# Kernel optimization log

Hardware: AMD Instinct MI355X
Metric: run time of the kernel (lower is better)

The kernel has to match this reference:

```python
import jax, jax.numpy as jnp
import numpy as np

B, S, D = 2, 2048, 1024
H, HD = 16, 64


def setup_inputs() -> dict:
    key = jax.random.key(0)
    ks = jax.random.split(key, 6)
    hidden_states = jax.random.normal(ks[0], (B, S, D), dtype=jnp.float32)
    c_attn_w = jax.random.normal(ks[1], (D, 3 * D), dtype=jnp.float32) * 0.02
    c_attn_b = jnp.zeros((3 * D,), dtype=jnp.float32)
    c_proj_w = jax.random.normal(ks[2], (D, D), dtype=jnp.float32) * 0.02
    c_proj_b = jnp.zeros((D,), dtype=jnp.float32)
    basis = jax.random.normal(ks[3], (H, HD, HD), dtype=jnp.float32) * 0.1
    projectors = jnp.einsum('hdr,her->hde', basis, basis)  # basis @ basis.T per head
    return {
        'hidden_states': hidden_states,
        'c_attn_w': c_attn_w,
        'c_attn_b': c_attn_b,
        'c_proj_w': c_proj_w,
        'c_proj_b': c_proj_b,
        'projectors': projectors,
    }


def reference(hidden_states, c_attn_w, c_attn_b, c_proj_w, c_proj_b, projectors):
    # GPT2 Conv1D: out = x @ W + b
    qkv = hidden_states @ c_attn_w + c_attn_b  # [B,S,3D]
    q, k, v = jnp.split(qkv, 3, axis=-1)
    # split heads -> [B,H,S,HD]
    def split_heads(t):
        return t.reshape(B, S, H, HD).transpose(0, 2, 1, 3)
    q, k, v = split_heads(q), split_heads(k), split_heads(v)
    scores = jnp.einsum('bhqd,bhkd->bhqk', q, k) / jnp.sqrt(jnp.float32(HD))
    causal = jnp.tril(jnp.ones((S, S), dtype=bool))
    scores = jnp.where(causal, scores, jnp.finfo(scores.dtype).min)
    probs = jax.nn.softmax(scores, axis=-1)
    attn = jnp.einsum('bhqk,bhkd->bhqd', probs, v)  # [B,H,S,HD]
    # per-head basis projector applied to attention output
    attn = jnp.einsum('bhsd,hde->bhse', attn, projectors)
    # merge heads -> [B,S,D]
    attn = attn.transpose(0, 2, 1, 3).reshape(B, S, D)
    out = attn @ c_proj_w + c_proj_b
    return out
```

## Files before the change

### kernel.cpp

```cpp
#include <hip/hip_runtime.h>

typedef __attribute__((ext_vector_type(8))) short bhalf8;
typedef __attribute__((ext_vector_type(4))) float f32x4;
typedef __attribute__((ext_vector_type(8))) unsigned short u16x8;
typedef __attribute__((ext_vector_type(4))) unsigned short u16x4;

#define BDIM 2
#define SDIM 2048
#define DDIM 1024
#define HDIM 16
#define HDHD 64

__device__ __forceinline__ unsigned short f2bf(float f) {
  unsigned u = __builtin_bit_cast(unsigned, f);
  u += 0x7fffu + ((u >> 16) & 1u);
  return (unsigned short)(u >> 16);
}

__global__ __launch_bounds__(256) void cvt_hidden(const float* __restrict__ x,
                                                  unsigned short* __restrict__ y) {
  size_t i = ((size_t)blockIdx.x * 256 + threadIdx.x) * 4;
  f32x4 v = *(const f32x4*)(x + i);
  u16x4 o;
  o[0] = f2bf(v[0]); o[1] = f2bf(v[1]); o[2] = f2bf(v[2]); o[3] = f2bf(v[3]);
  *(u16x4*)(y + i) = o;
}

__global__ __launch_bounds__(256) void transpose_cvt(const float* __restrict__ W,
                                                     unsigned short* __restrict__ Wt,
                                                     int R, int C) {
  __shared__ float tl[32][33];
  int rt = blockIdx.x * 32, ct = blockIdx.y * 32;
  int r8 = threadIdx.x >> 5, c = threadIdx.x & 31;
#pragma unroll
  for (int i = 0; i < 4; i++)
    tl[r8 + i * 8][c] = W[(size_t)(rt + r8 + i * 8) * C + ct + c];
  __syncthreads();
#pragma unroll
  for (int i = 0; i < 4; i++)
    Wt[(size_t)(ct + r8 + i * 8) * R + rt + c] = f2bf(tl[c][r8 + i * 8]);
}

__global__ __launch_bounds__(256) void make_wproj(const float* __restrict__ proj,
                                                  const float* __restrict__ wproj,
                                                  unsigned short* __restrict__ WT) {
  int h = blockIdx.x, ot = blockIdx.y * 64;
  __shared__ float Pl[64][65];
  __shared__ float Wl[64][65];
  int t = threadIdx.x;
#pragma unroll
  for (int i = 0; i < 16; i++) {
    int idx = t + 256 * i;
    int a = idx >> 6, bc = idx & 63;
    Pl[a][bc] = proj[(size_t)h * 4096 + idx];
    Wl[a][bc] = wproj[(size_t)(h * 64 + a) * 1024 + ot + bc];
  }
  __syncthreads();
  int d = t & 63, ob = t >> 6;
#pragma unroll
  for (int i = 0; i < 16; i++) {
    int o = ob + i * 4;
    float acc = 0.f;
#pragma unroll
    for (int e = 0; e < 64; e++) acc += Pl[d][e] * Wl[e][o];
    WT[(size_t)(ot + o) * 1024 + h * 64 + d] = f2bf(acc);
  }
}

template <int EPI>
__global__ __launch_bounds__(256) void gemm_bt(
    const unsigned short* __restrict__ A, const unsigned short* __restrict__ Bt,
    const float* __restrict__ bias, float* __restrict__ Cf,
    unsigned short* __restrict__ q, unsigned short* __restrict__ k,
    unsigned short* __restrict__ v, int M, int N, int K) {
  __shared__ unsigned short As[128][72];
  __shared__ unsigned short Bs[128][72];
  const int tid = threadIdx.x;
  const int m0 = blockIdx.y * 128, n0 = blockIdx.x * 128;
  f32x4 acc[4][4];
#pragma unroll
  for (int m = 0; m < 4; m++)
#pragma unroll
    for (int n = 0; n < 4; n++) acc[m][n] = f32x4{0.f, 0.f, 0.f, 0.f};
  const int w = tid >> 6, lane = tid & 63;
  const int wr = (w >> 1) * 64, wc = (w & 1) * 64;
  const int lrow = lane & 15, lk = (lane >> 4) * 8;

  for (int kt = 0; kt < K; kt += 64) {
    __syncthreads();
#pragma unroll
    for (int i = 0; i < 4; i++) {
      int cch = tid + 256 * i;
      int r = cch >> 3, c8 = cch & 7;
      *(u16x8*)(&As[r][c8 * 8]) = *(const u16x8*)(A + (size_t)(m0 + r) * K + kt + c8 * 8);
      *(u16x8*)(&Bs[r][c8 * 8]) = *(const u16x8*)(Bt + (size_t)(n0 + r) * K + kt + c8 * 8);
    }
    __syncthreads();
#pragma unroll
    for (int kk = 0; kk < 2; kk++) {
      bhalf8 af[4], bfr[4];
#pragma unroll
      for (int m = 0; m < 4; m++) af[m] = *(const bhalf8*)(&As[wr + m * 16 + lrow][kk * 32 + lk]);
#pragma unroll
      for (int n = 0; n < 4; n++) bfr[n] = *(const bhalf8*)(&Bs[wc + n * 16 + lrow][kk * 32 + lk]);
#pragma unroll
      for (int m = 0; m < 4; m++)
#pragma unroll
        for (int n = 0; n < 4; n++)
          acc[m][n] = __builtin_amdgcn_mfma_f32_16x16x32_bf16(af[m], bfr[n], acc[m][n], 0, 0, 0);
    }
  }
  const int g = lane >> 4, il = lane & 15;
#pragma unroll
  for (int m = 0; m < 4; m++) {
    int rowb = wr + m * 16 + 4 * g;
#pragma unroll
    for (int n = 0; n < 4; n++) {
      int col = n0 + wc + n * 16 + il;
      float bs = bias[col];
#pragma unroll
      for (int r = 0; r < 4; r++) {
        int row = m0 + rowb + r;
        float val = acc[m][n][r] + bs;
        if (EPI == 0) {
          int which = col >> 10, hh = (col >> 6) & 15, hd = col & 63;
          int b = row >> 11, s = row & 2047;
          size_t idx = ((size_t)(b * 16 + hh) * SDIM + s) * HDHD + hd;
          unsigned short bv = f2bf(which == 0 ? val * 0.1803368801f : val);
          if (which == 0) q[idx] = bv;
          else if (which == 1) k[idx] = bv;
          else v[idx] = bv;
        } else {
          Cf[(size_t)row * N + col] = val;
        }
      }
    }
  }
}

__global__ __launch_bounds__(128, 2) void attn_kernel(const unsigned short* __restrict__ Q,
                                                      const unsigned short* __restrict__ Kb,
                                                      const unsigned short* __restrict__ Vb,
                                                      unsigned short* __restrict__ Om) {
  __shared__ unsigned short Ks[64][72];
  __shared__ unsigned short Vt[64][72];
  __shared__ unsigned short Ps[2][32][72];
  const int bh = blockIdx.x;
  const int qt = 31 - blockIdx.y;
  const int tid = threadIdx.x;
  const int w = tid >> 6, lane = tid & 63;
  const int g = lane >> 4, il = lane & 15;
  const int qbase = qt * 64 + w * 32;
  const size_t bhS = (size_t)bh * SDIM;

  bhalf8 qf[2][2];
#pragma unroll
  for (int f = 0; f < 2; f++) {
    const unsigned short* qp = Q + (bhS + qbase + f * 16 + il) * HDHD + g * 8;
    qf[f][0] = *(const bhalf8*)(qp);
    qf[f][1] = *(const bhalf8*)(qp + 32);
  }
  f32x4 oacc[2][4];
#pragma unroll
  for (int f = 0; f < 2; f++)
#pragma unroll
    for (int i = 0; i < 4; i++) oacc[f][i] = f32x4{0.f, 0.f, 0.f, 0.f};
  float mrun[2] = {-1e30f, -1e30f}, lrun[2] = {0.f, 0.f};

  const int krow = tid >> 1;
  const int kchk = (tid & 1) * 32;
  const int vd0 = (tid & 31) * 2;
  const int vkg = (tid >> 5) * 16;
  const int nt = qt + 1;

  for (int kt = 0; kt < nt; kt++) {
    const size_t kbase = (bhS + (size_t)kt * 64) * HDHD;
    __syncthreads();
    {
      const unsigned short* src = Kb + kbase + krow * HDHD + kchk;
      *(u16x8*)(&Ks[krow][kchk]) = *(const u16x8*)(src);
      *(u16x8*)(&Ks[krow][kchk + 8]) = *(const u16x8*)(src + 8);
      *(u16x8*)(&Ks[krow][kchk + 16]) = *(const u16x8*)(src + 16);
      *(u16x8*)(&Ks[krow][kchk + 24]) = *(const u16x8*)(src + 24);
    }
    {
      const unsigned short* vsrc = Vb + kbase + (size_t)vkg * HDHD + vd0;
      u16x8 lo0, lo1, hi0, hi1;
#pragma unroll
      for (int i = 0; i < 8; i++) {
        unsigned vv = *(const unsigned*)(vsrc + i * HDHD);
        lo0[i] = (unsigned short)(vv & 0xffffu); hi0[i] = (unsigned short)(vv >> 16);
      }
#pragma unroll
      for (int i = 0; i < 8; i++) {
        unsigned vv = *(const unsigned*)(vsrc + (8 + i) * HDHD);
        lo1[i] = (unsigned short)(vv & 0xffffu); hi1[i] = (unsigned short)(vv >> 16);
      }
      *(u16x8*)(&Vt[vd0][vkg]) = lo0;     *(u16x8*)(&Vt[vd0][vkg + 8]) = lo1;
      *(u16x8*)(&Vt[vd0 + 1][vkg]) = hi0; *(u16x8*)(&Vt[vd0 + 1][vkg + 8]) = hi1;
    }
    __syncthreads();
    f32x4 s[2][4];
#pragma unroll
    for (int f = 0; f < 2; f++)
#pragma unroll
      for (int c = 0; c < 4; c++) s[f][c] = f32x4{0.f, 0.f, 0.f, 0.f};
#pragma unroll
    for (int c = 0; c < 4; c++) {
      bhalf8 kf0 = *(const bhalf8*)(&Ks[c * 16 + il][g * 8]);
      bhalf8 kf1 = *(const bhalf8*)(&Ks[c * 16 + il][32 + g * 8]);
#pragma unroll
      for (int f = 0; f < 2; f++) {
        s[f][c] = __builtin_amdgcn_mfma_f32_16x16x32_bf16(kf0, qf[f][0], s[f][c], 0, 0, 0);
        s[f][c] = __builtin_amdgcn_mfma_f32_16x16x32_bf16(kf1, qf[f][1], s[f][c], 0, 0, 0);
      }
    }
    const bool diag = (kt == qt);
#pragma unroll
    for (int f = 0; f < 2; f++) {
      const int thr = w * 32 + f * 16 + il;
      float p[4][4];
      float lmax = -1e30f;
#pragma unroll
      for (int c = 0; c < 4; c++)
#pragma unroll
        for (int r = 0; r < 4; r++) {
          float v = s[f][c][r];
          if (diag && (c * 16 + 4 * g + r > thr)) v = -1e30f;
          p[c][r] = v;
          lmax = fmaxf(lmax, v);
        }
      lmax = fmaxf(lmax, __shfl_xor(lmax, 16));
      lmax = fmaxf(lmax, __shfl_xor(lmax, 32));
      float mn = fmaxf(mrun[f], lmax);
      float sc = exp2f(mrun[f] - mn);
      mrun[f] = mn;
      float rs = 0.f;
#pragma unroll
      for (int c = 0; c < 4; c++)
#pragma unroll
        for (int r = 0; r < 4; r++) { p[c][r] = exp2f(p[c][r] - mn); rs += p[c][r]; }
      rs += __shfl_xor(rs, 16);
      rs += __shfl_xor(rs, 32);
      lrun[f] = lrun[f] * sc + rs;
#pragma unroll
      for (int df = 0; df < 4; df++)
#pragma unroll
        for (int r = 0; r < 4; r++) oacc[f][df][r] *= sc;
#pragma unroll
      for (int c = 0; c < 4; c++) {
        u16x4 pk;
#pragma unroll
        for (int r = 0; r < 4; r++) pk[r] = f2bf(p[c][r]);
        *(u16x4*)(&Ps[w][f * 16 + il][c * 16 + 4 * g]) = pk;
      }
    }
#pragma unroll
    for (int kk = 0; kk < 2; kk++) {
      bhalf8 pf0 = *(const bhalf8*)(&Ps[w][il][kk * 32 + g * 8]);
      bhalf8 pf1 = *(const bhalf8*)(&Ps[w][16 + il][kk * 32 + g * 8]);
#pragma unroll
      for (int df = 0; df < 4; df++) {
        bhalf8 vf = *(const bhalf8*)(&Vt[df * 16 + il][kk * 32 + g * 8]);
        oacc[0][df] = __builtin_amdgcn_mfma_f32_16x16x32_bf16(vf, pf0, oacc[0][df], 0, 0, 0);
        oacc[1][df] = __builtin_amdgcn_mfma_f32_16x16x32_bf16(vf, pf1, oacc[1][df], 0, 0, 0);
      }
    }
  }
  __syncthreads();
#pragma unroll
  for (int f = 0; f < 2; f++) {
    float inv = 1.f / lrun[f];
#pragma unroll
    for (int df = 0; df < 4; df++) {
      u16x4 o;
#pragma unroll
      for (int r = 0; r < 4; r++) o[r] = f2bf(oacc[f][df][r] * inv);
      *(u16x4*)(&Ks[w * 32 + f * 16 + il][df * 16 + 4 * g]) = o;
    }
  }
  __syncthreads();
  {
    const int row = tid >> 1, half = (tid & 1) * 32;
    const int b = bh >> 4, h = bh & 15;
    size_t obase = ((size_t)b * SDIM + qt * 64 + row) * DDIM + h * HDHD + half;
#pragma unroll
    for (int c8 = 0; c8 < 4; c8++)
      *(u16x8*)(Om + obase + c8 * 8) = *(const u16x8*)(&Ks[row][half + c8 * 8]);
  }
}

extern "C" void kernel_launch(void* const* d_in, const int* in_sizes, int n_in,
                              void* d_out, int out_size, void* d_ws, size_t ws_size,
                              hipStream_t stream) {
  const float* hidden = (const float*)d_in[0];
  const float* attn_w = (const float*)d_in[1];
  const float* attn_b = (const float*)d_in[2];
  const float* proj_w = (const float*)d_in[3];
  const float* proj_b = (const float*)d_in[4];
  const float* projectors = (const float*)d_in[5];
  float* out = (float*)d_out;
  char* ws = (char*)d_ws;
  (void)in_sizes; (void)n_in; (void)out_size; (void)ws_size;

  unsigned short* hseq   = (unsigned short*)(ws);
  unsigned short* wqkvT  = (unsigned short*)(ws + 8388608);
  unsigned short* qb     = (unsigned short*)(ws + 14680064);
  unsigned short* kb     = (unsigned short*)(ws + 23068672);
  unsigned short* vb     = (unsigned short*)(ws + 31457280);
  unsigned short* attnM  = (unsigned short*)(ws + 39845888);
  unsigned short* wprojT = (unsigned short*)(ws + 48234496);

  cvt_hidden<<<dim3(4096), dim3(256), 0, stream>>>(hidden, hseq);
  transpose_cvt<<<dim3(32, 96), dim3(256), 0, stream>>>(attn_w, wqkvT, 1024, 3072);
  make_wproj<<<dim3(16, 16), dim3(256), 0, stream>>>(projectors, proj_w, wprojT);
  gemm_bt<0><<<dim3(24, 32), dim3(256), 0, stream>>>(hseq, wqkvT, attn_b, nullptr,
                                                     qb, kb, vb, 4096, 3072, 1024);
  attn_kernel<<<dim3(32, 32), dim3(128), 0, stream>>>(qb, kb, vb, attnM);
  gemm_bt<1><<<dim3(8, 32), dim3(256), 0, stream>>>(attnM, wprojT, proj_b, out,
                                                    nullptr, nullptr, nullptr, 4096, 1024, 1024);
}
```

Baseline: 177.2 us.

## Split causal attention over key segments with a separate reduction pass

Attention is split along the key dimension into segments of 8 key tiles, launched as a 3D grid, so the long diagonal query tiles no longer dominate and the workload is balanced across CUs. Each segment writes bf16 partial outputs with per-row max/sum, and a new reduce kernel combines them. The partial kernel also prefetches the next K/V tile into registers and raises the occupancy hint. The cost is an extra launch, a workspace round-trip, and bf16 rounding of the partials; the old single-pass kernel remains as a fallback when the workspace is too small.

```diff
diff --git a/kernel.cpp b/kernel.cpp
--- a/kernel.cpp
+++ b/kernel.cpp
@@ -15,6 +15,9 @@
   unsigned u = __builtin_bit_cast(unsigned, f);
   u += 0x7fffu + ((u >> 16) & 1u);
   return (unsigned short)(u >> 16);
+}
+__device__ __forceinline__ float bf2f(unsigned short u) {
+  return __builtin_bit_cast(float, (unsigned)u << 16);
 }
 
 __global__ __launch_bounds__(256) void cvt_hidden(const float* __restrict__ x,
@@ -138,7 +141,237 @@
   }
 }
 
-__global__ __launch_bounds__(128, 2) void attn_kernel(const unsigned short* __restrict__ Q,
+__global__ __launch_bounds__(128, 3) void attn_partial(const unsigned short* __restrict__ Q,
+                                                       const unsigned short* __restrict__ Kb,
+                                                       const unsigned short* __restrict__ Vb,
+                                                       unsigned short* __restrict__ PO,
+                                                       float2* __restrict__ ML) {
+  __shared__ unsigned short Ks[64][72];
+  __shared__ unsigned short Vt[64][72];
+  __shared__ unsigned short Ps[2][32][72];
+  const int bh = blockIdx.x;
+  const int qt = 31 - blockIdx.y;
+  const int seg = blockIdx.z;
+  const int a = qt >> 3, bq = qt & 7;
+  const int nseg = a + 1;
+  if (seg >= nseg) return;
+  const int k0 = seg * 8;
+  const int k1 = min(k0 + 8, qt + 1);
+
+  const int tid = threadIdx.x;
+  const int w = tid >> 6, lane = tid & 63;
+  const int g = lane >> 4, il = lane & 15;
+  const int qbase = qt * 64 + w * 32;
+  const size_t bhS = (size_t)bh * SDIM;
+
+  bhalf8 qf[2][2];
+#pragma unroll
+  for (int f = 0; f < 2; f++) {
+    const unsigned short* qp = Q + (bhS + qbase + f * 16 + il) * HDHD + g * 8;
+    qf[f][0] = *(const bhalf8*)(qp);
+    qf[f][1] = *(const bhalf8*)(qp + 32);
+  }
+  f32x4 oacc[2][4];
+#pragma unroll
+  for (int f = 0; f < 2; f++)
+#pragma unroll
+    for (int i = 0; i < 4; i++) oacc[f][i] = f32x4{0.f, 0.f, 0.f, 0.f};
+  float mrun[2] = {-1e30f, -1e30f}, lrun[2] = {0.f, 0.f};
+
+  const int krow = tid >> 1;
+  const int kchk = (tid & 1) * 32;
+  const int vd0 = (tid & 31) * 2;
+  const int vkg = (tid >> 5) * 16;
+
+  u16x8 kr[4];
+  unsigned vr[16];
+  {
+    const size_t kb0 = (bhS + (size_t)k0 * 64) * HDHD;
+    const unsigned short* ksrc = Kb + kb0 + krow * HDHD + kchk;
+#pragma unroll
+    for (int i = 0; i < 4; i++) kr[i] = *(const u16x8*)(ksrc + i * 8);
+    const unsigned short* vsrc = Vb + kb0 + (size_t)vkg * HDHD + vd0;
+#pragma unroll
+    for (int i = 0; i < 16; i++) vr[i] = *(const unsigned*)(vsrc + i * HDHD);
+  }
+
+  for (int kt = k0; kt < k1; kt++) {
+    __syncthreads();
+#pragma unroll
+    for (int i = 0; i < 4; i++) *(u16x8*)(&Ks[krow][kchk + i * 8]) = kr[i];
+    {
+      u16x8 lo0, lo1, hi0, hi1;
+#pragma unroll
+      for (int i = 0; i < 8; i++) {
+        lo0[i] = (unsigned short)(vr[i] & 0xffffu); hi0[i] = (unsigned short)(vr[i] >> 16);
+      }
+#pragma unroll
+      for (int i = 0; i < 8; i++) {
+        lo1[i] = (unsigned short)(vr[8 + i] & 0xffffu); hi1[i] = (unsigned short)(vr[8 + i] >> 16);
+      }
+      *(u16x8*)(&Vt[vd0][vkg]) = lo0;     *(u16x8*)(&Vt[vd0][vkg + 8]) = lo1;
+      *(u16x8*)(&Vt[vd0 + 1][vkg]) = hi0; *(u16x8*)(&Vt[vd0 + 1][vkg + 8]) = hi1;
+    }
+    if (kt + 1 < k1) {
+      const size_t kbn = (bhS + (size_t)(kt + 1) * 64) * HDHD;
+      const unsigned short* ksrc = Kb + kbn + krow * HDHD + kchk;
+#pragma unroll
+      for (int i = 0; i < 4; i++) kr[i] = *(const u16x8*)(ksrc + i * 8);
+      const unsigned short* vsrc = Vb + kbn + (size_t)vkg * HDHD + vd0;
+#pragma unroll
+      for (int i = 0; i < 16; i++) vr[i] = *(const unsigned*)(vsrc + i * HDHD);
+    }
+    __syncthreads();
+    f32x4 s[2][4];
+#pragma unroll
+    for (int f = 0; f < 2; f++)
+#pragma unroll
+      for (int c = 0; c < 4; c++) s[f][c] = f32x4{0.f, 0.f, 0.f, 0.f};
+#pragma unroll
+    for (int c = 0; c < 4; c++) {
+      bhalf8 kf0 = *(const bhalf8*)(&Ks[c * 16 + il][g * 8]);
+      bhalf8 kf1 = *(const bhalf8*)(&Ks[c * 16 + il][32 + g * 8]);
+#pragma unroll
+      for (int f = 0; f < 2; f++) {
+        s[f][c] = __builtin_amdgcn_mfma_f32_16x16x32_bf16(kf0, qf[f][0], s[f][c], 0, 0, 0);
+        s[f][c] = __builtin_amdgcn_mfma_f32_16x16x32_bf16(kf1, qf[f][1], s[f][c], 0, 0, 0);
+      }
+    }
+    const bool diag = (kt == qt);
+    float lmax[2];
+#pragma unroll
+    for (int f = 0; f < 2; f++) {
+      const int thr = w * 32 + f * 16 + il;
+      float lm = -1e30f;
+#pragma unroll
+      for (int c = 0; c < 4; c++)
+#pragma unroll
+        for (int r = 0; r < 4; r++) {
+          float v = s[f][c][r];
+          if (diag && (c * 16 + 4 * g + r > thr)) v = -1e30f;
+          s[f][c][r] = v;
+          lm = fmaxf(lm, v);
+        }
+      lm = fmaxf(lm, __shfl_xor(lm, 16));
+      lm = fmaxf(lm, __shfl_xor(lm, 32));
+      lmax[f] = lm;
+    }
+    if (!__all((lmax[0] <= mrun[0] + 7.f) && (lmax[1] <= mrun[1] + 7.f))) {
+#pragma unroll
+      for (int f = 0; f < 2; f++) {
+        float mn = fmaxf(mrun[f], lmax[f]);
+        float sc = exp2f(mrun[f] - mn);
+        mrun[f] = mn;
+        lrun[f] *= sc;
+#pragma unroll
+        for (int df = 0; df < 4; df++)
+#pragma unroll
+          for (int r = 0; r < 4; r++) oacc[f][df][r] *= sc;
+      }
+    }
+#pragma unroll
+    for (int f = 0; f < 2; f++) {
+      float rs = 0.f;
+#pragma unroll
+      for (int c = 0; c < 4; c++) {
+        u16x4 pk;
+#pragma unroll
+        for (int r = 0; r < 4; r++) {
+          float pv = exp2f(s[f][c][r] - mrun[f]);
+          rs += pv;
+          pk[r] = f2bf(pv);
+        }
+        *(u16x4*)(&Ps[w][f * 16 + il][c * 16 + 4 * g]) = pk;
+      }
+      rs += __shfl_xor(rs, 16);
+      rs += __shfl_xor(rs, 32);
+      lrun[f] += rs;
+    }
+#pragma unroll
+    for (int kk = 0; kk < 2; kk++) {
+      bhalf8 pf0 = *(const bhalf8*)(&Ps[w][il][kk * 32 + g * 8]);
+      bhalf8 pf1 = *(const bhalf8*)(&Ps[w][16 + il][kk * 32 + g * 8]);
+#pragma unroll
+      for (int df = 0; df < 4; df++) {
+        bhalf8 vf = *(const bhalf8*)(&Vt[df * 16 + il][kk * 32 + g * 8]);
+        oacc[0][df] = __builtin_amdgcn_mfma_f32_16x16x32_bf16(vf, pf0, oacc[0][df], 0, 0, 0);
+        oacc[1][df] = __builtin_amdgcn_mfma_f32_16x16x32_bf16(vf, pf1, oacc[1][df], 0, 0, 0);
+      }
+    }
+  }
+  const int pidx = bh * 80 + 4 * a * (a + 1) + bq * (a + 1) + seg;
+  __syncthreads();
+#pragma unroll
+  for (int f = 0; f < 2; f++) {
+    float inv = 1.f / lrun[f];
+#pragma unroll
+    for (int df = 0; df < 4; df++) {
+      u16x4 o;
+#pragma unroll
+      for (int r = 0; r < 4; r++) o[r] = f2bf(oacc[f][df][r] * inv);
+      *(u16x4*)(&Ks[w * 32 + f * 16 + il][df * 16 + 4 * g]) = o;
+    }
+  }
+  if (g == 0) {
+#pragma unroll
+    for (int f = 0; f < 2; f++)
+      ML[(size_t)pidx * 64 + w * 32 + f * 16 + il] = make_float2(mrun[f], lrun[f]);
+  }
+  __syncthreads();
+  {
+    const int row = tid >> 1, half = (tid & 1) * 32;
+    unsigned short* dst = PO + (size_t)pidx * 4096 + (size_t)row * 64 + half;
+#pragma unroll
+    for (int c8 = 0; c8 < 4; c8++)
+      *(u16x8*)(dst + c8 * 8) = *(const u16x8*)(&Ks[row][half + c8 * 8]);
+  }
+}
+
+__global__ __launch_bounds__(256) void attn_reduce(const unsigned short* __restrict__ PO,
+                                                   const float2* __restrict__ ML,
+                                                   unsigned short* __restrict__ Om) {
+  const int bh = blockIdx.x, qt = blockIdx.y;
+  const int a = qt >> 3, bq = qt & 7;
+  const int nseg = a + 1;
+  const int base = bh * 80 + 4 * a * (a + 1) + bq * (a + 1);
+  const int t = threadIdx.x;
+  const int r = t >> 2, dc = (t & 3) * 16;
+  float2 mls[4];
+  float M = -1e30f;
+#pragma unroll
+  for (int s = 0; s < 4; s++) {
+    if (s < nseg) { mls[s] = ML[(size_t)(base + s) * 64 + r]; M = fmaxf(M, mls[s].x); }
+  }
+  float L = 0.f;
+  float O[16];
+#pragma unroll
+  for (int j = 0; j < 16; j++) O[j] = 0.f;
+#pragma unroll
+  for (int s = 0; s < 4; s++) {
+    if (s < nseg) {
+      float wgt = mls[s].y * exp2f(mls[s].x - M);
+      L += wgt;
+      const unsigned short* p = PO + (size_t)(base + s) * 4096 + r * 64 + dc;
+      u16x8 p0 = *(const u16x8*)p, p1 = *(const u16x8*)(p + 8);
+#pragma unroll
+      for (int j = 0; j < 8; j++) O[j] += wgt * bf2f(p0[j]);
+#pragma unroll
+      for (int j = 0; j < 8; j++) O[8 + j] += wgt * bf2f(p1[j]);
+    }
+  }
+  float inv = 1.f / L;
+  const int b = bh >> 4, h = bh & 15;
+  size_t orow = ((size_t)b * SDIM + qt * 64 + r) * DDIM + h * HDHD + dc;
+  u16x8 o0, o1;
+#pragma unroll
+  for (int j = 0; j < 8; j++) o0[j] = f2bf(O[j] * inv);
+#pragma unroll
+  for (int j = 0; j < 8; j++) o1[j] = f2bf(O[8 + j] * inv);
+  *(u16x8*)(Om + orow) = o0;
+  *(u16x8*)(Om + orow + 8) = o1;
+}
+
+__global__ __launch_bounds__(128, 2) void attn_direct(const unsigned short* __restrict__ Q,
                                                       const unsigned short* __restrict__ Kb,
                                                       const unsigned short* __restrict__ Vb,
                                                       unsigned short* __restrict__ Om) {
@@ -152,7 +385,6 @@
   const int g = lane >> 4, il = lane & 15;
   const int qbase = qt * 64 + w * 32;
   const size_t bhS = (size_t)bh * SDIM;
-
   bhalf8 qf[2][2];
 #pragma unroll
   for (int f = 0; f < 2; f++) {
@@ -166,22 +398,16 @@
 #pragma unroll
     for (int i = 0; i < 4; i++) oacc[f][i] = f32x4{0.f, 0.f, 0.f, 0.f};
   float mrun[2] = {-1e30f, -1e30f}, lrun[2] = {0.f, 0.f};
-
-  const int krow = tid >> 1;
-  const int kchk = (tid & 1) * 32;
-  const int vd0 = (tid & 31) * 2;
-  const int vkg = (tid >> 5) * 16;
+  const int krow = tid >> 1, kchk = (tid & 1) * 32;
+  const int vd0 = (tid & 31) * 2, vkg = (tid >> 5) * 16;
   const int nt = qt + 1;
-
   for (int kt = 0; kt < nt; kt++) {
     const size_t kbase = (bhS + (size_t)kt * 64) * HDHD;
     __syncthreads();
     {
       const unsigned short* src = Kb + kbase + krow * HDHD + kchk;
-      *(u16x8*)(&Ks[krow][kchk]) = *(const u16x8*)(src);
-      *(u16x8*)(&Ks[krow][kchk + 8]) = *(const u16x8*)(src + 8);
-      *(u16x8*)(&Ks[krow][kchk + 16]) = *(const u16x8*)(src + 16);
-      *(u16x8*)(&Ks[krow][kchk + 24]) = *(const u16x8*)(src + 24);
+#pragma unroll
+      for (int i = 0; i < 4; i++) *(u16x8*)(&Ks[krow][kchk + i * 8]) = *(const u16x8*)(src + i * 8);
     }
     {
       const unsigned short* vsrc = Vb + kbase + (size_t)vkg * HDHD + vd0;
@@ -301,7 +527,7 @@
   const float* projectors = (const float*)d_in[5];
   float* out = (float*)d_out;
   char* ws = (char*)d_ws;
-  (void)in_sizes; (void)n_in; (void)out_size; (void)ws_size;
+  (void)in_sizes; (void)n_in; (void)out_size;
 
   unsigned short* hseq   = (unsigned short*)(ws);
   unsigned short* wqkvT  = (unsigned short*)(ws + 8388608);
@@ -310,13 +536,21 @@
   unsigned short* vb     = (unsigned short*)(ws + 31457280);
   unsigned short* attnM  = (unsigned short*)(ws + 39845888);
   unsigned short* wprojT = (unsigned short*)(ws + 48234496);
+  unsigned short* PO     = (unsigned short*)(ws + 50331648);
+  float2*         ML2    = (float2*)(ws + 71303168);
+  const size_t ws_needed = 71303168 + 1310720;
 
   cvt_hidden<<<dim3(4096), dim3(256), 0, stream>>>(hidden, hseq);
   transpose_cvt<<<dim3(32, 96), dim3(256), 0, stream>>>(attn_w, wqkvT, 1024, 3072);
   make_wproj<<<dim3(16, 16), dim3(256), 0, stream>>>(projectors, proj_w, wprojT);
   gemm_bt<0><<<dim3(24, 32), dim3(256), 0, stream>>>(hseq, wqkvT, attn_b, nullptr,
                                                      qb, kb, vb, 4096, 3072, 1024);
-  attn_kernel<<<dim3(32, 32), dim3(128), 0, stream>>>(qb, kb, vb, attnM);
+  if (ws_size >= ws_needed) {
+    attn_partial<<<dim3(32, 32, 4), dim3(128), 0, stream>>>(qb, kb, vb, PO, ML2);
+    attn_reduce<<<dim3(32, 32), dim3(256), 0, stream>>>(PO, ML2, attnM);
+  } else {
+    attn_direct<<<dim3(32, 32), dim3(128), 0, stream>>>(qb, kb, vb, attnM);
+  }
   gemm_bt<1><<<dim3(8, 32), dim3(256), 0, stream>>>(attnM, wprojT, proj_b, out,
                                                     nullptr, nullptr, nullptr, 4096, 1024, 1024);
 }
```

Result: faster. 171.7 us (-3.1%).
